# Kernel optimization log

Measured on AMD Instinct MI355X. Metric: run time of the kernel, lower is better.

The kernel has to match this reference:

```python
import jax, jax.numpy as jnp
import numpy as np

N_NODES = 50000
N_EDGES = 800000
EMBED_ROWS = 100000
NUM_RELS = 16
NUM_BASES = 4
FEAT_DIM = 32
OUT_DIM = 32
ATTN_DIM = 32


def setup_inputs() -> dict:
    key = jax.random.key(0)
    ks = jax.random.split(key, 16)
    inp = {
        'feat': jax.random.normal(ks[0], (N_NODES, FEAT_DIM), jnp.float32),
        'embed_table': jax.random.normal(ks[1], (EMBED_ROWS, FEAT_DIM), jnp.float32),
        'transform': jax.random.normal(ks[2], (FEAT_DIM * 2, OUT_DIM), jnp.float32) * 0.1,
        'weight': jax.random.normal(ks[3], (NUM_BASES, OUT_DIM, OUT_DIM), jnp.float32) * 0.1,
        'w_comp': jax.random.normal(ks[4], (NUM_RELS, NUM_BASES), jnp.float32) * 0.5,
        'self_loop_weight': jax.random.normal(ks[5], (OUT_DIM, OUT_DIM), jnp.float32) * 0.1,
        'A_w': jax.random.normal(ks[6], (2 * OUT_DIM + ATTN_DIM, OUT_DIM), jnp.float32) * 0.1,
        'A_b': jax.random.normal(ks[7], (OUT_DIM,), jnp.float32) * 0.1,
        'B_w': jax.random.normal(ks[8], (OUT_DIM, 1), jnp.float32) * 0.1,
        'B_b': jax.random.normal(ks[9], (1,), jnp.float32) * 0.1,
        'attn_emb': jax.random.normal(ks[10], (NUM_RELS, ATTN_DIM), jnp.float32),
        'idx': jax.random.randint(ks[11], (N_NODES,), 0, EMBED_ROWS, jnp.int32),
        'edge_src': jax.random.randint(ks[12], (N_EDGES,), 0, N_NODES, jnp.int32),
        'edge_dst': jax.random.randint(ks[13], (N_EDGES,), 0, N_NODES, jnp.int32),
        'edge_type': jax.random.randint(ks[14], (N_EDGES,), 0, NUM_RELS, jnp.int32),
    }
    return inp


def reference(feat, embed_table, transform, weight, w_comp, self_loop_weight,
              A_w, A_b, B_w, B_b, attn_emb, idx, edge_src, edge_dst, edge_type):
    n = feat.shape[0]
    # input-layer features: concat(feat, embed[idx]) @ transform -> init_fea [N, D]
    init_fea = jnp.concatenate([feat, embed_table[idx]], axis=1) @ transform
    # basis decomposition: rel_w [R, D, D]
    rel_w = jnp.einsum('rb,bio->rio', w_comp, weight)
    # per-edge gather (is_input_layer & add_transe_emb -> x=src init_fea, y=dst init_fea)
    x = init_fea[edge_src]                      # [E, D]
    y = init_fea[edge_dst]                      # [E, D]
    w_e = rel_w[edge_type]                      # [E, D, D]
    msg = jnp.einsum('ed,edo->eo', x, w_e)      # per-edge bmm (edge weight w = 1)
    # attention MLP: a = sigmoid(B(relu(A([x, y, rel_emb]))))
    e = jnp.concatenate([x, y, attn_emb[edge_type]], axis=1)  # [E, 2D+A]
    a = jax.nn.sigmoid(jax.nn.relu(e @ A_w + A_b) @ B_w + B_b)  # [E, 1]
    # scatter-reduce: h_v = curr_emb_v + sum_{e: dst=v} a_e * msg_e
    agg = jax.ops.segment_sum(a * msg, edge_dst, num_segments=n)
    curr = init_fea @ self_loop_weight
    h = jax.nn.relu(curr + agg)  # activation=relu, bias=None, dropout=0
    # is_input_layer & add_transe_emb: repr = concat(init_fea, h) -> [N, 2, D]
    return jnp.stack([init_fea, h], axis=1)
```

## Files before the change

### kernel.cpp

```cpp
#include <hip/hip_runtime.h>
#include <math.h>

#define NN 50000
#define NE 800000
#define NR 16
#define NEP_MAX (NE + NR * 16)
#define NB 196
#define NBIN 212
#define ABLK 256
#define CHUNK ((NE + ABLK - 1) / ABLK)

typedef __attribute__((ext_vector_type(8))) short short8;
typedef __attribute__((ext_vector_type(4))) float floatx4;

__device__ __forceinline__ unsigned short f2bf(float x) {
    unsigned int u = __float_as_uint(x);
    u += 0x7fffu + ((u >> 16) & 1u);
    return (unsigned short)(u >> 16);
}
__device__ __forceinline__ float bf2f(unsigned short s) {
    return __uint_as_float(((unsigned int)s) << 16);
}

__global__ void k_prep(const float* __restrict__ weight, const float* __restrict__ w_comp,
                       const float* __restrict__ A_w, const float* __restrict__ A_b,
                       const float* __restrict__ attn_emb,
                       unsigned short* __restrict__ wfrag, unsigned short* __restrict__ afrag,
                       float* __restrict__ aproj) {
    int g = blockIdx.x * blockDim.x + threadIdx.x;
    if (g < 16 * 2 * 64 * 8) {
        int t = g >> 10, rest = g & 1023;
        int nt = rest >> 9, l = (rest >> 3) & 63, j = rest & 7;
        int k = (l >> 4) * 8 + j, n = (l & 15) + 16 * nt;
        float acc = 0.f;
#pragma unroll
        for (int b = 0; b < 4; b++) acc += w_comp[t * 4 + b] * weight[b * 1024 + k * 32 + n];
        wfrag[g] = f2bf(acc);
    }
    if (g < 2 * 2 * 64 * 8) {
        int ks = g >> 10, rest = g & 1023;
        int nt = rest >> 9, l = (rest >> 3) & 63, j = rest & 7;
        int k = ks * 32 + (l >> 4) * 8 + j, n = (l & 15) + 16 * nt;
        afrag[g] = f2bf(A_w[k * 32 + n]);
    }
    if (g < 16 * 32) {
        int t = g >> 5, j = g & 31;
        float acc = A_b[j];
#pragma unroll
        for (int k = 0; k < 32; k++) acc += attn_emb[t * 32 + k] * A_w[(64 + k) * 32 + j];
        aproj[g] = acc;
    }
}

__global__ void k_init(const float* __restrict__ feat, const float* __restrict__ emb,
                       const float* __restrict__ T, const int* __restrict__ idx,
                       float* __restrict__ out, unsigned short* __restrict__ init_bf) {
    int i = blockIdx.x * blockDim.x + threadIdx.x;
    if (i >= NN) return;
    float v[32], acc[32];
#pragma unroll
    for (int o = 0; o < 32; o++) acc[o] = 0.f;
    const float4* fp = (const float4*)(feat + (size_t)i * 32);
#pragma unroll
    for (int q = 0; q < 8; q++) {
        float4 f = fp[q];
        v[4 * q] = f.x; v[4 * q + 1] = f.y; v[4 * q + 2] = f.z; v[4 * q + 3] = f.w;
    }
#pragma unroll
    for (int d = 0; d < 32; d++) {
        float xd = v[d];
#pragma unroll
        for (int o = 0; o < 32; o++) acc[o] += xd * T[d * 32 + o];
    }
    int row = idx[i];
    const float4* ep = (const float4*)(emb + (size_t)row * 32);
#pragma unroll
    for (int q = 0; q < 8; q++) {
        float4 f = ep[q];
        v[4 * q] = f.x; v[4 * q + 1] = f.y; v[4 * q + 2] = f.z; v[4 * q + 3] = f.w;
    }
#pragma unroll
    for (int d = 0; d < 32; d++) {
        float xd = v[d];
#pragma unroll
        for (int o = 0; o < 32; o++) acc[o] += xd * T[(32 + d) * 32 + o];
    }
    float4* op = (float4*)(out + (size_t)i * 64);
#pragma unroll
    for (int q = 0; q < 8; q++) {
        float4 f;
        f.x = acc[4 * q]; f.y = acc[4 * q + 1]; f.z = acc[4 * q + 2]; f.w = acc[4 * q + 3];
        op[q] = f;
    }
    unsigned int w[16];
#pragma unroll
    for (int q = 0; q < 16; q++)
        w[q] = (unsigned int)f2bf(acc[2 * q]) | ((unsigned int)f2bf(acc[2 * q + 1]) << 16);
    uint4* bp = (uint4*)(init_bf + (size_t)i * 32);
#pragma unroll
    for (int q = 0; q < 4; q++) {
        uint4 u; u.x = w[4 * q]; u.y = w[4 * q + 1]; u.z = w[4 * q + 2]; u.w = w[4 * q + 3];
        bp[q] = u;
    }
}

__global__ void __launch_bounds__(256) k_count(const int* __restrict__ ed,
                                               const int* __restrict__ et,
                                               int* __restrict__ cpb) {
    __shared__ int lc[NBIN];
    for (int i = threadIdx.x; i < NBIN; i += 256) lc[i] = 0;
    __syncthreads();
    const int start = blockIdx.x * CHUNK, end = min(start + CHUNK, NE);
    for (int e = start + threadIdx.x; e < end; e += 256) {
        atomicAdd(&lc[ed[e] >> 8], 1);
        atomicAdd(&lc[NB + et[e]], 1);
    }
    __syncthreads();
    for (int i = threadIdx.x; i < NBIN; i += 256) cpb[blockIdx.x * NBIN + i] = lc[i];
}

__global__ void __launch_bounds__(256) k_scanB(int* __restrict__ cpb,
                                               int* __restrict__ boff,
                                               int* __restrict__ toff,
                                               int* __restrict__ tend) {
    __shared__ int tot[NBIN];
    int bin = threadIdx.x;
    if (bin < NBIN) {
        int run = 0;
        for (int c = 0; c < ABLK; c++) {
            int v = cpb[c * NBIN + bin];
            cpb[c * NBIN + bin] = run;
            run += v;
        }
        tot[bin] = run;
    }
    __syncthreads();
    if (threadIdx.x == 0) {
        int acc = 0;
        for (int b = 0; b < NB; b++) { boff[b] = acc; acc += tot[b]; }
        boff[NB] = acc;
        int t0 = 0;
        for (int t = 0; t < NR; t++) {
            toff[t] = t0;
            tend[t] = t0 + tot[NB + t];
            t0 += ((tot[NB + t] + 15) >> 4) << 4;
        }
        toff[NR] = t0;
    }
}

__global__ void __launch_bounds__(256) k_scatA(const int* __restrict__ es,
                                               const int* __restrict__ ed,
                                               const int* __restrict__ et,
                                               const int* __restrict__ cpb,
                                               const int* __restrict__ boff,
                                               const int* __restrict__ toff,
                                               int* __restrict__ tsrc,
                                               int* __restrict__ tdst,
                                               int* __restrict__ bpack) {
    __shared__ int cur[NBIN];
    const int start = blockIdx.x * CHUNK, end = min(start + CHUNK, NE);
    for (int i = threadIdx.x; i < NBIN; i += 256) {
        int base = (i < NB) ? boff[i] : toff[i - NB];
        cur[i] = base + cpb[blockIdx.x * NBIN + i];
    }
    __syncthreads();
    for (int e = start + threadIdx.x; e < end; e += 256) {
        int s = es[e], d = ed[e], t = et[e];
        int q = atomicAdd(&cur[NB + t], 1);
        int slot = atomicAdd(&cur[d >> 8], 1);
        tsrc[q] = s;
        tdst[q] = d;
        bpack[slot] = (q << 8) | (d & 255);
    }
}

__global__ void __launch_bounds__(256) k_fine(const int* __restrict__ boff,
                                              const int* __restrict__ bpack,
                                              int* __restrict__ row_off,
                                              int* __restrict__ p_of_q) {
    __shared__ int h[256], ls[256];
    const int b = blockIdx.x;
    const int s0 = boff[b], s1 = boff[b + 1];
    const int tid = threadIdx.x;
    h[tid] = 0;
    __syncthreads();
    for (int s = s0 + tid; s < s1; s += 256)
        atomicAdd(&h[bpack[s] & 255], 1);
    __syncthreads();
    int v = h[tid];
    ls[tid] = v;
    __syncthreads();
    for (int off = 1; off < 256; off <<= 1) {
        int t = (tid >= off) ? ls[tid - off] : 0;
        __syncthreads();
        ls[tid] += t;
        __syncthreads();
    }
    int excl = ls[tid] - v;
    int node = b * 256 + tid;
    if (node <= NN) row_off[node] = s0 + excl;
    h[tid] = s0 + excl;
    __syncthreads();
    for (int s = s0 + tid; s < s1; s += 256) {
        int pk = bpack[s];
        int p = atomicAdd(&h[pk & 255], 1);
        p_of_q[pk >> 8] = p;
    }
}

__global__ void __launch_bounds__(256) k_msg(
    const unsigned short* __restrict__ wfrag, const unsigned short* __restrict__ afrag,
    const float* __restrict__ aproj, const float* __restrict__ B_w,
    const float* __restrict__ B_b, const int* __restrict__ toff,
    const int* __restrict__ tend, const int* __restrict__ tsrc,
    const int* __restrict__ tdst, const int* __restrict__ p_of_q,
    const unsigned short* __restrict__ init_bf, unsigned short* __restrict__ amsg) {
    const int wave = threadIdx.x >> 6;
    const int lane = threadIdx.x & 63;
    const int q0 = (blockIdx.x * 4 + wave) * 16;
    if (q0 >= toff[NR]) return;
    int t = 0;
#pragma unroll
    for (int i = 1; i < NR; i++) t += (q0 >= toff[i]) ? 1 : 0;
    t = __builtin_amdgcn_readfirstlane(t);
    const int te = tend[t];
    const int m = lane & 15, quad = lane >> 4;
    const int qa = q0 + m;
    const bool va = qa < te;
    int src = va ? tsrc[qa] : 0;
    int dst = va ? tdst[qa] : 0;
    short8 xa = *(const short8*)(init_bf + (size_t)src * 32 + quad * 8);
    short8 ya = *(const short8*)(init_bf + (size_t)dst * 32 + quad * 8);
    short8 wb0 = *(const short8*)(wfrag + (size_t)((t * 2 + 0) * 64 + lane) * 8);
    short8 wb1 = *(const short8*)(wfrag + (size_t)((t * 2 + 1) * 64 + lane) * 8);
    short8 a00 = *(const short8*)(afrag + (size_t)((0 * 2 + 0) * 64 + lane) * 8);
    short8 a01 = *(const short8*)(afrag + (size_t)((0 * 2 + 1) * 64 + lane) * 8);
    short8 a10 = *(const short8*)(afrag + (size_t)((1 * 2 + 0) * 64 + lane) * 8);
    short8 a11 = *(const short8*)(afrag + (size_t)((1 * 2 + 1) * 64 + lane) * 8);
    floatx4 z4 = {0.f, 0.f, 0.f, 0.f};
    floatx4 mc0 = __builtin_amdgcn_mfma_f32_16x16x32_bf16(xa, wb0, z4, 0, 0, 0);
    floatx4 mc1 = __builtin_amdgcn_mfma_f32_16x16x32_bf16(xa, wb1, z4, 0, 0, 0);
    floatx4 hc0 = __builtin_amdgcn_mfma_f32_16x16x32_bf16(xa, a00, z4, 0, 0, 0);
    hc0 = __builtin_amdgcn_mfma_f32_16x16x32_bf16(ya, a10, hc0, 0, 0, 0);
    floatx4 hc1 = __builtin_amdgcn_mfma_f32_16x16x32_bf16(xa, a01, z4, 0, 0, 0);
    hc1 = __builtin_amdgcn_mfma_f32_16x16x32_bf16(ya, a11, hc1, 0, 0, 0);
    const int col = m;
    float ap0 = aproj[t * 32 + col], ap1 = aproj[t * 32 + 16 + col];
    float bw0 = B_w[col], bw1 = B_w[col + 16];
    float bb = B_b[0];
    float part[4];
#pragma unroll
    for (int r = 0; r < 4; r++)
        part[r] = fmaxf(hc0[r] + ap0, 0.f) * bw0 + fmaxf(hc1[r] + ap1, 0.f) * bw1;
#pragma unroll
    for (int s = 1; s < 16; s <<= 1) {
#pragma unroll
        for (int r = 0; r < 4; r++) part[r] += __shfl_xor(part[r], s, 64);
    }
#pragma unroll
    for (int r = 0; r < 4; r++) {
        int qe = q0 + quad * 4 + r;
        if (qe < te) {
            int pe = p_of_q[qe];
            float a = 1.f / (1.f + __expf(-(part[r] + bb)));
            amsg[(size_t)pe * 32 + col] = f2bf(a * mc0[r]);
            amsg[(size_t)pe * 32 + col + 16] = f2bf(a * mc1[r]);
        }
    }
}

__global__ void __launch_bounds__(256) k_agg(
    const int* __restrict__ row_off, const unsigned short* __restrict__ amsg,
    const float* __restrict__ S, float* __restrict__ out) {
    int tid = threadIdx.x;
    int v = blockIdx.x * 64 + (tid >> 2);
    if (v >= NN) return;
    int c0 = (tid & 3) * 8;
    float acc[8];
#pragma unroll
    for (int j = 0; j < 8; j++) acc[j] = 0.f;
    int p0 = row_off[v], p1 = row_off[v + 1];
    for (int p = p0; p < p1; p++) {
        short8 mv = *(const short8*)(amsg + (size_t)p * 32 + c0);
#pragma unroll
        for (int j = 0; j < 8; j++) acc[j] += bf2f((unsigned short)mv[j]);
    }
    float x[32];
    const float4* xp = (const float4*)(out + (size_t)v * 64);
#pragma unroll
    for (int q = 0; q < 8; q++) {
        float4 f = xp[q];
        x[4 * q] = f.x; x[4 * q + 1] = f.y; x[4 * q + 2] = f.z; x[4 * q + 3] = f.w;
    }
#pragma unroll
    for (int d = 0; d < 32; d++) {
        float xd = x[d];
#pragma unroll
        for (int j = 0; j < 8; j++) acc[j] += xd * S[d * 32 + c0 + j];
    }
    float4* op = (float4*)(out + (size_t)v * 64 + 32 + c0);
#pragma unroll
    for (int q = 0; q < 2; q++) {
        float4 f;
        f.x = fmaxf(acc[4 * q], 0.f);
        f.y = fmaxf(acc[4 * q + 1], 0.f);
        f.z = fmaxf(acc[4 * q + 2], 0.f);
        f.w = fmaxf(acc[4 * q + 3], 0.f);
        op[q] = f;
    }
}

extern "C" void kernel_launch(void* const* d_in, const int* in_sizes, int n_in,
                              void* d_out, int out_size, void* d_ws, size_t ws_size,
                              hipStream_t stream) {
    const float* feat      = (const float*)d_in[0];
    const float* embed     = (const float*)d_in[1];
    const float* transform = (const float*)d_in[2];
    const float* weight    = (const float*)d_in[3];
    const float* w_comp    = (const float*)d_in[4];
    const float* self_w    = (const float*)d_in[5];
    const float* A_w       = (const float*)d_in[6];
    const float* A_b       = (const float*)d_in[7];
    const float* B_w       = (const float*)d_in[8];
    const float* B_b       = (const float*)d_in[9];
    const float* attn_emb  = (const float*)d_in[10];
    const int*   idx       = (const int*)d_in[11];
    const int*   edge_src  = (const int*)d_in[12];
    const int*   edge_dst  = (const int*)d_in[13];
    const int*   edge_type = (const int*)d_in[14];
    float* out = (float*)d_out;

    char* ws = (char*)d_ws;
    unsigned short* amsg    = (unsigned short*)ws;
    int*            bpack   = (int*)ws;
    unsigned short* init_bf = (unsigned short*)(ws + (size_t)NEP_MAX * 64);
    unsigned short* wfrag   = (unsigned short*)((char*)init_bf + 3200000);
    unsigned short* afrag   = (unsigned short*)((char*)wfrag + 32768);
    float*          aproj   = (float*)((char*)afrag + 4096);
    int* ip       = (int*)((char*)aproj + 2048);
    int* toff     = ip;              ip += 32;
    int* tend     = ip;              ip += 16;
    int* boff     = ip;              ip += 200;
    int* cpb      = ip;              ip += ABLK * NBIN;
    int* row_off  = ip;              ip += NN + 1;
    int* tsrc     = ip;              ip += NEP_MAX;
    int* tdst     = ip;              ip += NEP_MAX;
    int* p_of_q   = ip;              ip += NEP_MAX;

    k_prep<<<(16384 + 255) / 256, 256, 0, stream>>>(weight, w_comp, A_w, A_b, attn_emb,
                                                    wfrag, afrag, aproj);
    k_init<<<(NN + 255) / 256, 256, 0, stream>>>(feat, embed, transform, idx, out, init_bf);
    k_count<<<ABLK, 256, 0, stream>>>(edge_dst, edge_type, cpb);
    k_scanB<<<1, 256, 0, stream>>>(cpb, boff, toff, tend);
    k_scatA<<<ABLK, 256, 0, stream>>>(edge_src, edge_dst, edge_type, cpb, boff, toff,
                                      tsrc, tdst, bpack);
    k_fine<<<NB, 256, 0, stream>>>(boff, bpack, row_off, p_of_q);
    const int tiles = NEP_MAX / 16;
    k_msg<<<(tiles + 3) / 4, 256, 0, stream>>>(wfrag, afrag, aproj, B_w, B_b,
                                               toff, tend, tsrc, tdst, p_of_q,
                                               init_bf, amsg);
    k_agg<<<(NN + 63) / 64, 256, 0, stream>>>(row_off, amsg, self_w, out);
}
```

Measured before the change: 212.6 us.

## Merge prep and init kernels, widen count/scatter blocks to 1024 threads

Fuses the weight-prep and node-init kernels into one launch, with the first 64 blocks doing the prep work, which removes one kernel launch and its dependency gap. The count and scatter kernels move from 256 to 1024 threads per block for more memory-level parallelism per chunk. The scan now writes exclusive offsets to a separate buffer with an unrolled loop instead of overwriting in place. Shared-memory atomic contention per block rises with the larger blocks, and the 1024-thread blocks are a register-pressure risk.

```diff
diff --git a/kernel.cpp b/kernel.cpp
--- a/kernel.cpp
+++ b/kernel.cpp
@@ -22,40 +22,41 @@
     return __uint_as_float(((unsigned int)s) << 16);
 }
 
-__global__ void k_prep(const float* __restrict__ weight, const float* __restrict__ w_comp,
-                       const float* __restrict__ A_w, const float* __restrict__ A_b,
-                       const float* __restrict__ attn_emb,
-                       unsigned short* __restrict__ wfrag, unsigned short* __restrict__ afrag,
-                       float* __restrict__ aproj) {
-    int g = blockIdx.x * blockDim.x + threadIdx.x;
-    if (g < 16 * 2 * 64 * 8) {
-        int t = g >> 10, rest = g & 1023;
-        int nt = rest >> 9, l = (rest >> 3) & 63, j = rest & 7;
-        int k = (l >> 4) * 8 + j, n = (l & 15) + 16 * nt;
-        float acc = 0.f;
-#pragma unroll
-        for (int b = 0; b < 4; b++) acc += w_comp[t * 4 + b] * weight[b * 1024 + k * 32 + n];
-        wfrag[g] = f2bf(acc);
-    }
-    if (g < 2 * 2 * 64 * 8) {
-        int ks = g >> 10, rest = g & 1023;
-        int nt = rest >> 9, l = (rest >> 3) & 63, j = rest & 7;
-        int k = ks * 32 + (l >> 4) * 8 + j, n = (l & 15) + 16 * nt;
-        afrag[g] = f2bf(A_w[k * 32 + n]);
-    }
-    if (g < 16 * 32) {
-        int t = g >> 5, j = g & 31;
-        float acc = A_b[j];
-#pragma unroll
-        for (int k = 0; k < 32; k++) acc += attn_emb[t * 32 + k] * A_w[(64 + k) * 32 + j];
-        aproj[g] = acc;
-    }
-}
-
-__global__ void k_init(const float* __restrict__ feat, const float* __restrict__ emb,
-                       const float* __restrict__ T, const int* __restrict__ idx,
-                       float* __restrict__ out, unsigned short* __restrict__ init_bf) {
-    int i = blockIdx.x * blockDim.x + threadIdx.x;
+__global__ void k_pre(const float* __restrict__ feat, const float* __restrict__ emb,
+                      const float* __restrict__ T, const int* __restrict__ idx,
+                      const float* __restrict__ weight, const float* __restrict__ w_comp,
+                      const float* __restrict__ A_w, const float* __restrict__ A_b,
+                      const float* __restrict__ attn_emb,
+                      float* __restrict__ out, unsigned short* __restrict__ init_bf,
+                      unsigned short* __restrict__ wfrag, unsigned short* __restrict__ afrag,
+                      float* __restrict__ aproj) {
+    if (blockIdx.x < 64) {
+        int g = blockIdx.x * 256 + threadIdx.x;
+        {
+            int t = g >> 10, rest = g & 1023;
+            int nt = rest >> 9, l = (rest >> 3) & 63, j = rest & 7;
+            int k = (l >> 4) * 8 + j, n = (l & 15) + 16 * nt;
+            float acc = 0.f;
+#pragma unroll
+            for (int b = 0; b < 4; b++) acc += w_comp[t * 4 + b] * weight[b * 1024 + k * 32 + n];
+            wfrag[g] = f2bf(acc);
+        }
+        if (g < 2 * 2 * 64 * 8) {
+            int ks = g >> 10, rest = g & 1023;
+            int nt = rest >> 9, l = (rest >> 3) & 63, j = rest & 7;
+            int k = ks * 32 + (l >> 4) * 8 + j, n = (l & 15) + 16 * nt;
+            afrag[g] = f2bf(A_w[k * 32 + n]);
+        }
+        if (g < 16 * 32) {
+            int t = g >> 5, j = g & 31;
+            float acc = A_b[j];
+#pragma unroll
+            for (int k = 0; k < 32; k++) acc += attn_emb[t * 32 + k] * A_w[(64 + k) * 32 + j];
+            aproj[g] = acc;
+        }
+        return;
+    }
+    int i = (blockIdx.x - 64) * 256 + threadIdx.x;
     if (i >= NN) return;
     float v[32], acc[32];
 #pragma unroll
@@ -104,22 +105,23 @@
     }
 }
 
-__global__ void __launch_bounds__(256) k_count(const int* __restrict__ ed,
-                                               const int* __restrict__ et,
-                                               int* __restrict__ cpb) {
+__global__ void __launch_bounds__(1024) k_count(const int* __restrict__ ed,
+                                                const int* __restrict__ et,
+                                                int* __restrict__ cpb) {
     __shared__ int lc[NBIN];
-    for (int i = threadIdx.x; i < NBIN; i += 256) lc[i] = 0;
+    for (int i = threadIdx.x; i < NBIN; i += 1024) lc[i] = 0;
     __syncthreads();
     const int start = blockIdx.x * CHUNK, end = min(start + CHUNK, NE);
-    for (int e = start + threadIdx.x; e < end; e += 256) {
+    for (int e = start + threadIdx.x; e < end; e += 1024) {
         atomicAdd(&lc[ed[e] >> 8], 1);
         atomicAdd(&lc[NB + et[e]], 1);
     }
     __syncthreads();
-    for (int i = threadIdx.x; i < NBIN; i += 256) cpb[blockIdx.x * NBIN + i] = lc[i];
-}
-
-__global__ void __launch_bounds__(256) k_scanB(int* __restrict__ cpb,
+    for (int i = threadIdx.x; i < NBIN; i += 1024) cpb[blockIdx.x * NBIN + i] = lc[i];
+}
+
+__global__ void __launch_bounds__(256) k_scanB(const int* __restrict__ cpb,
+                                               int* __restrict__ cpbx,
                                                int* __restrict__ boff,
                                                int* __restrict__ toff,
                                                int* __restrict__ tend) {
@@ -127,9 +129,10 @@
     int bin = threadIdx.x;
     if (bin < NBIN) {
         int run = 0;
+#pragma unroll 8
         for (int c = 0; c < ABLK; c++) {
             int v = cpb[c * NBIN + bin];
-            cpb[c * NBIN + bin] = run;
+            cpbx[c * NBIN + bin] = run;
             run += v;
         }
         tot[bin] = run;
@@ -149,23 +152,23 @@
     }
 }
 
-__global__ void __launch_bounds__(256) k_scatA(const int* __restrict__ es,
-                                               const int* __restrict__ ed,
-                                               const int* __restrict__ et,
-                                               const int* __restrict__ cpb,
-                                               const int* __restrict__ boff,
-                                               const int* __restrict__ toff,
-                                               int* __restrict__ tsrc,
-                                               int* __restrict__ tdst,
-                                               int* __restrict__ bpack) {
+__global__ void __launch_bounds__(1024) k_scatA(const int* __restrict__ es,
+                                                const int* __restrict__ ed,
+                                                const int* __restrict__ et,
+                                                const int* __restrict__ cpbx,
+                                                const int* __restrict__ boff,
+                                                const int* __restrict__ toff,
+                                                int* __restrict__ tsrc,
+                                                int* __restrict__ tdst,
+                                                int* __restrict__ bpack) {
     __shared__ int cur[NBIN];
     const int start = blockIdx.x * CHUNK, end = min(start + CHUNK, NE);
-    for (int i = threadIdx.x; i < NBIN; i += 256) {
+    for (int i = threadIdx.x; i < NBIN; i += 1024) {
         int base = (i < NB) ? boff[i] : toff[i - NB];
-        cur[i] = base + cpb[blockIdx.x * NBIN + i];
-    }
-    __syncthreads();
-    for (int e = start + threadIdx.x; e < end; e += 256) {
+        cur[i] = base + cpbx[blockIdx.x * NBIN + i];
+    }
+    __syncthreads();
+    for (int e = start + threadIdx.x; e < end; e += 1024) {
         int s = es[e], d = ed[e], t = et[e];
         int q = atomicAdd(&cur[NB + t], 1);
         int slot = atomicAdd(&cur[d >> 8], 1);
@@ -343,18 +346,18 @@
     int* tend     = ip;              ip += 16;
     int* boff     = ip;              ip += 200;
     int* cpb      = ip;              ip += ABLK * NBIN;
+    int* cpbx     = ip;              ip += ABLK * NBIN;
     int* row_off  = ip;              ip += NN + 1;
     int* tsrc     = ip;              ip += NEP_MAX;
     int* tdst     = ip;              ip += NEP_MAX;
     int* p_of_q   = ip;              ip += NEP_MAX;
 
-    k_prep<<<(16384 + 255) / 256, 256, 0, stream>>>(weight, w_comp, A_w, A_b, attn_emb,
-                                                    wfrag, afrag, aproj);
-    k_init<<<(NN + 255) / 256, 256, 0, stream>>>(feat, embed, transform, idx, out, init_bf);
-    k_count<<<ABLK, 256, 0, stream>>>(edge_dst, edge_type, cpb);
-    k_scanB<<<1, 256, 0, stream>>>(cpb, boff, toff, tend);
-    k_scatA<<<ABLK, 256, 0, stream>>>(edge_src, edge_dst, edge_type, cpb, boff, toff,
-                                      tsrc, tdst, bpack);
+    k_pre<<<260, 256, 0, stream>>>(feat, embed, transform, idx, weight, w_comp,
+                                   A_w, A_b, attn_emb, out, init_bf, wfrag, afrag, aproj);
+    k_count<<<ABLK, 1024, 0, stream>>>(edge_dst, edge_type, cpb);
+    k_scanB<<<1, 256, 0, stream>>>(cpb, cpbx, boff, toff, tend);
+    k_scatA<<<ABLK, 1024, 0, stream>>>(edge_src, edge_dst, edge_type, cpbx, boff, toff,
+                                       tsrc, tdst, bpack);
     k_fine<<<NB, 256, 0, stream>>>(boff, bpack, row_off, p_of_q);
     const int tiles = NEP_MAX / 16;
     k_msg<<<(tiles + 3) / 4, 256, 0, stream>>>(wfrag, afrag, aproj, B_w, B_b,
```

Result: no change. 214.4 us (+0.9%).
